# Performance work log

Measured on AMD Instinct MI355X. Metric: run time of the kernel, lower is better.

## Reference

```python
import jax, jax.numpy as jnp
import numpy as np

ALPHA = 0.2  # LeakyReLU negative slope

def setup_inputs() -> dict:
    key = jax.random.key(0)
    kx, kw, kb, ka = jax.random.split(key, 4)
    B, K, D, H = 4, 256, 128, 4
    x = jax.random.normal(kx, (B, K, D), dtype=jnp.float32)
    # Per-head Linear(2D -> D): stored as (H, 2D, D), i.e. transposed torch layout (y = v @ W + b)
    W = jax.random.normal(kw, (H, 2 * D, D), dtype=jnp.float32) * (1.0 / np.sqrt(2 * D))
    lin_b = jax.random.normal(kb, (H, D), dtype=jnp.float32) * 0.01
    # Per-head attention vector a: (H, D)
    a = jax.random.normal(ka, (H, D), dtype=jnp.float32) * (1.0 / np.sqrt(D))
    # Per-head additive bias over attention logits, initialized to zeros like the torch module
    bias = jnp.zeros((H, K, K), dtype=jnp.float32)
    return {"x": x, "W": W, "lin_b": lin_b, "a": a, "bias": bias}

def reference(x, W, lin_b, a, bias):
    # GATv2, dense all-pairs attention over K nodes, eval mode (dropout off).
    # Faithful decomposition: Linear(concat(x_i, x_j)) == x_i @ W_src + x_j @ W_dst + b
    B, K, D = x.shape
    H = W.shape[0]
    outs = []
    for h in range(H):  # small fixed head count; each head has distinct params
        W_src, W_dst = W[h, :D], W[h, D:]          # (D, D) each
        left = x @ W_src                            # (B, K, D) -> contribution of node i
        right = x @ W_dst                           # (B, K, D) -> contribution of node j
        s = left[:, :, None, :] + right[:, None, :, :] + lin_b[h]  # (B, K, K, D)
        s = jnp.where(s > 0, s, ALPHA * s)          # LeakyReLU
        e = jnp.einsum('bijd,d->bij', s, a[h]) + bias[h]           # (B, K, K)
        attn = jax.nn.softmax(e, axis=2)
        outs.append(attn @ x)                       # (B, K, D)
    return jnp.mean(jnp.stack(outs, axis=-1), axis=-1)
```

## Files before the change

kernel.cpp:

```cpp
#include <hip/hip_runtime.h>
#include <math.h>

constexpr int Kc = 256, Dc = 128, Mc = 1024;

typedef _Float16 h2_t __attribute__((ext_vector_type(2)));
union U32H2 { unsigned int u; h2_t h; };
__device__ inline h2_t u2h(unsigned int u) { U32H2 x; x.u = u; return x.h; }
__device__ inline unsigned int h2u(h2_t h) { U32H2 x; x.h = h; return x.u; }
__device__ inline unsigned int packh(float a, float b) {
    h2_t h; h.x = (_Float16)a; h.y = (_Float16)b; return h2u(h);
}
__device__ inline unsigned int f2bf(float f) {
    unsigned int u = __float_as_uint(f);
    return (u + 0x7FFFu + ((u >> 16) & 1u)) >> 16;
}
__device__ inline float bf2f_lo(unsigned int u) { return __uint_as_float(u << 16); }
__device__ inline float bf2f_hi(unsigned int u) { return __uint_as_float(u & 0xFFFF0000u); }

__device__ inline float estep(unsigned int r, unsigned int l, h2_t av, float acc) {
    h2_t s = u2h(r) + u2h(l);
    unsigned int t = h2u(s) & 0x7FFF7FFFu;
#if __has_builtin(__builtin_amdgcn_fdot2)
    return __builtin_amdgcn_fdot2(u2h(t), av, acc, false);
#else
    h2_t th = u2h(t);
    return fmaf((float)th.x, (float)av.x, fmaf((float)th.y, (float)av.y, acc));
#endif
}

__global__ __launch_bounds__(256) void k1(const float* __restrict__ x,
                                          const float* __restrict__ W,
                                          const float* __restrict__ lin_b,
                                          const float* __restrict__ a,
                                          unsigned int* __restrict__ Lpp,
                                          unsigned int* __restrict__ Rtp,
                                          float* __restrict__ eb) {
    __shared__ float As[128][32];
    __shared__ float Bs[128][64];
    __shared__ float red[4][16][4];

    const int tid = threadIdx.x;
    const int bid = blockIdx.x;
    const int tx = tid & 15, ty = tid >> 4;
    const bool isL = (bid < 256);

    int h, b, m0, n0, dt;
    if (isL) {
        const int nt = bid & 1, mt = (bid >> 1) & 31;
        h = (bid >> 6) & 3;
        m0 = mt * 32; n0 = nt * 64; b = 0; dt = 0;
        {
            const int m_l = tid & 31, kq = tid >> 5;
            #pragma unroll
            for (int c = 0; c < 4; ++c) {
                const int k0 = kq * 16 + c * 4;
                const float4 v = *(const float4*)&x[(m0 + m_l) * Dc + k0];
                As[k0 + 0][m_l] = v.x; As[k0 + 1][m_l] = v.y;
                As[k0 + 2][m_l] = v.z; As[k0 + 3][m_l] = v.w;
            }
        }
        {
            const int n_l = tid & 63, kq = tid >> 6;
            const float* Wb = W + (h * 2) * Dc * Dc;
            #pragma unroll
            for (int kk = 0; kk < 32; ++kk) {
                const int k = kq * 32 + kk;
                Bs[k][n_l] = Wb[k * Dc + n0 + n_l];
            }
        }
    } else {
        const int r_ = bid - 256;
        const int jt = r_ & 3;
        dt = (r_ >> 2) & 3;
        b  = (r_ >> 4) & 3;
        h  = (r_ >> 6) & 3;
        m0 = dt * 32;
        n0 = jt * 64;
        {
            const int d_l = tid & 31, kq = tid >> 5;
            const float* Wb = W + ((h * 2 + 1) * Dc) * Dc;
            #pragma unroll
            for (int kk = 0; kk < 16; ++kk) {
                const int k = kq * 16 + kk;
                As[k][d_l] = Wb[k * Dc + m0 + d_l];
            }
        }
        {
            const int j_l = tid & 63, kq = tid >> 6;
            #pragma unroll
            for (int c = 0; c < 8; ++c) {
                const int k0 = kq * 32 + c * 4;
                const float4 v = *(const float4*)&x[(b * Kc + n0 + j_l) * Dc + k0];
                Bs[k0 + 0][j_l] = v.x; Bs[k0 + 1][j_l] = v.y;
                Bs[k0 + 2][j_l] = v.z; Bs[k0 + 3][j_l] = v.w;
            }
        }
    }
    __syncthreads();

    float acc[2][4];
    #pragma unroll
    for (int r = 0; r < 2; ++r)
        #pragma unroll
        for (int c = 0; c < 4; ++c) acc[r][c] = 0.f;

    #pragma unroll 16
    for (int k = 0; k < 128; ++k) {
        const float2 xa = *(const float2*)&As[k][ty * 2];
        const float4 wb = *(const float4*)&Bs[k][tx * 4];
        acc[0][0] = fmaf(xa.x, wb.x, acc[0][0]);
        acc[0][1] = fmaf(xa.x, wb.y, acc[0][1]);
        acc[0][2] = fmaf(xa.x, wb.z, acc[0][2]);
        acc[0][3] = fmaf(xa.x, wb.w, acc[0][3]);
        acc[1][0] = fmaf(xa.y, wb.x, acc[1][0]);
        acc[1][1] = fmaf(xa.y, wb.y, acc[1][1]);
        acc[1][2] = fmaf(xa.y, wb.z, acc[1][2]);
        acc[1][3] = fmaf(xa.y, wb.w, acc[1][3]);
    }

    if (isL) {
        const float4 lv = *(const float4*)&lin_b[h * Dc + n0 + tx * 4];
        #pragma unroll
        for (int r = 0; r < 2; ++r) {
            uint2 pk;
            pk.x = packh(acc[r][0] + lv.x, acc[r][1] + lv.y);
            pk.y = packh(acc[r][2] + lv.z, acc[r][3] + lv.w);
            *(uint2*)&Lpp[(h * Mc + m0 + ty * 2 + r) * 64 + (n0 >> 1) + tx * 2] = pk;
        }
    } else {
        {
            uint4 pk;
            pk.x = packh(acc[0][0], acc[1][0]);
            pk.y = packh(acc[0][1], acc[1][1]);
            pk.z = packh(acc[0][2], acc[1][2]);
            pk.w = packh(acc[0][3], acc[1][3]);
            *(uint4*)&Rtp[((h * 4 + b) * 64 + (m0 >> 1) + ty) * Kc + n0 + tx * 4] = pk;
        }
        const float2 av = *(const float2*)&a[h * Dc + m0 + ty * 2];
        float p0 = 0.4f * (av.x * acc[0][0] + av.y * acc[1][0]);
        float p1 = 0.4f * (av.x * acc[0][1] + av.y * acc[1][1]);
        float p2 = 0.4f * (av.x * acc[0][2] + av.y * acc[1][2]);
        float p3 = 0.4f * (av.x * acc[0][3] + av.y * acc[1][3]);
        p0 += __shfl_xor(p0, 16, 64); p0 += __shfl_xor(p0, 32, 64);
        p1 += __shfl_xor(p1, 16, 64); p1 += __shfl_xor(p1, 32, 64);
        p2 += __shfl_xor(p2, 16, 64); p2 += __shfl_xor(p2, 32, 64);
        p3 += __shfl_xor(p3, 16, 64); p3 += __shfl_xor(p3, 32, 64);
        if (((tid >> 4) & 3) == 0) {
            const int w = tid >> 6;
            red[w][tx][0] = p0; red[w][tx][1] = p1;
            red[w][tx][2] = p2; red[w][tx][3] = p3;
        }
        __syncthreads();
        if (tid < 64) {
            const int txl = tid >> 2, c = tid & 3;
            const float v = red[0][txl][c] + red[1][txl][c] + red[2][txl][c] + red[3][txl][c];
            eb[((h * 4 + b) * 4 + dt) * Kc + n0 + tid] = 1.5f * v;
        }
    }
}

__global__ __launch_bounds__(256) void k2(const float* __restrict__ a,
                                          const float* __restrict__ bias,
                                          const unsigned int* __restrict__ Lpp,
                                          const unsigned int* __restrict__ Rtp,
                                          const float* __restrict__ eb,
                                          unsigned short* __restrict__ Pws) {
    __shared__ float red[256 * 20];
    __shared__ unsigned int lpT2[64 * 4];
    __shared__ unsigned int aa2s[64];

    const int tid = threadIdx.x;
    const int L = blockIdx.x;
    const int xcd = L & 7, q = L >> 3;
    const int hb = (xcd << 1) | (q & 1);
    const int it = q >> 1;
    const int h = hb >> 2, b = hb & 3;
    const int i0 = it * 4;

    {
        const int i = tid & 3, dp = tid >> 2;
        lpT2[dp * 4 + i] = Lpp[(h * Mc + b * Kc + i0 + i) * 64 + dp];
    }
    if (tid < 64) aa2s[tid] = packh(0.4f * a[h * Dc + 2 * tid], 0.4f * a[h * Dc + 2 * tid + 1]);
    __syncthreads();

    const int dq = tid >> 6, j4 = tid & 63;
    float4 acc0 = make_float4(0.f, 0.f, 0.f, 0.f);
    float4 acc1 = make_float4(0.f, 0.f, 0.f, 0.f);
    float4 acc2 = make_float4(0.f, 0.f, 0.f, 0.f);
    float4 acc3 = make_float4(0.f, 0.f, 0.f, 0.f);
    {
        const unsigned int* rb = Rtp + (hb * 64 + dq * 16) * Kc + j4 * 4;
        const unsigned int* lt = lpT2 + dq * 16 * 4;
        const unsigned int* at = aa2s + dq * 16;
        #pragma unroll
        for (int dp = 0; dp < 16; ++dp) {
            const uint4 rr = *(const uint4*)(rb + dp * Kc);
            const uint4 lp = *(const uint4*)(lt + dp * 4);
            const h2_t av = u2h(at[dp]);
            acc0.x = estep(rr.x, lp.x, av, acc0.x);
            acc0.y = estep(rr.y, lp.x, av, acc0.y);
            acc0.z = estep(rr.z, lp.x, av, acc0.z);
            acc0.w = estep(rr.w, lp.x, av, acc0.w);
            acc1.x = estep(rr.x, lp.y, av, acc1.x);
            acc1.y = estep(rr.y, lp.y, av, acc1.y);
            acc1.z = estep(rr.z, lp.y, av, acc1.z);
            acc1.w = estep(rr.w, lp.y, av, acc1.w);
            acc2.x = estep(rr.x, lp.z, av, acc2.x);
            acc2.y = estep(rr.y, lp.z, av, acc2.y);
            acc2.z = estep(rr.z, lp.z, av, acc2.z);
            acc2.w = estep(rr.w, lp.z, av, acc2.w);
            acc3.x = estep(rr.x, lp.w, av, acc3.x);
            acc3.y = estep(rr.y, lp.w, av, acc3.y);
            acc3.z = estep(rr.z, lp.w, av, acc3.z);
            acc3.w = estep(rr.w, lp.w, av, acc3.w);
        }
    }
    {
        float* myred = red + tid * 20;
        *(float4*)&myred[0]  = acc0;
        *(float4*)&myred[4]  = acc1;
        *(float4*)&myred[8]  = acc2;
        *(float4*)&myred[12] = acc3;
    }
    __syncthreads();

    {
        const int w = tid >> 6, l = tid & 63;
        float4 e0 = make_float4(0.f, 0.f, 0.f, 0.f);
        #pragma unroll
        for (int q4 = 0; q4 < 4; ++q4) {
            const float4 v = *(const float4*)&red[(q4 * 64 + l) * 20 + w * 4];
            e0.x += v.x; e0.y += v.y; e0.z += v.z; e0.w += v.w;
        }
        float4 ebs = make_float4(0.f, 0.f, 0.f, 0.f);
        #pragma unroll
        for (int seg = 0; seg < 4; ++seg) {
            const float4 v = *(const float4*)&eb[(hb * 4 + seg) * Kc + l * 4];
            ebs.x += v.x; ebs.y += v.y; ebs.z += v.z; ebs.w += v.w;
        }
        const float4 bv = *(const float4*)&bias[(h * Kc + i0 + w) * Kc + l * 4];
        e0.x += ebs.x + bv.x;
        e0.y += ebs.y + bv.y;
        e0.z += ebs.z + bv.z;
        e0.w += ebs.w + bv.w;

        float m = fmaxf(fmaxf(e0.x, e0.y), fmaxf(e0.z, e0.w));
        #pragma unroll
        for (int off = 1; off < 64; off <<= 1) m = fmaxf(m, __shfl_xor(m, off, 64));
        const float p0 = __expf(e0.x - m), p1 = __expf(e0.y - m);
        const float p2 = __expf(e0.z - m), p3 = __expf(e0.w - m);
        float s = p0 + p1 + p2 + p3;
        #pragma unroll
        for (int off = 1; off < 64; off <<= 1) s += __shfl_xor(s, off, 64);
        const float sc = 0.25f / s;
        uint2 pk;
        pk.x = f2bf(p0 * sc) | (f2bf(p1 * sc) << 16);
        pk.y = f2bf(p2 * sc) | (f2bf(p3 * sc) << 16);
        *(uint2*)&Pws[(hb * Kc + i0 + w) * Kc + l * 4] = pk;
    }
}

__global__ __launch_bounds__(256) void k3(const float* __restrict__ x,
                                          const unsigned short* __restrict__ Pws,
                                          float* __restrict__ out) {
    __shared__ float pbar[2 * Kc];
    __shared__ float red[256 * 12];

    const int tid = threadIdx.x;
    const int bid = blockIdx.x;
    const int b = bid >> 7, it = bid & 127;
    const int i0 = it * 2;

    if (tid < 128) {
        const int r = tid >> 6, c = tid & 63;
        float4 s = make_float4(0.f, 0.f, 0.f, 0.f);
        #pragma unroll
        for (int h = 0; h < 4; ++h) {
            const uint2 v = *(const uint2*)&Pws[((h * 4 + b) * Kc + i0 + r) * Kc + c * 4];
            s.x += bf2f_lo(v.x); s.y += bf2f_hi(v.x);
            s.z += bf2f_lo(v.y); s.w += bf2f_hi(v.y);
        }
        *(float4*)&pbar[r * Kc + c * 4] = s;
    }
    __syncthreads();

    const int jq = tid >> 5, dd4 = tid & 31;
    float4 o0 = make_float4(0.f, 0.f, 0.f, 0.f);
    float4 o1 = make_float4(0.f, 0.f, 0.f, 0.f);
    {
        const float* xb = x + (b * Kc) * Dc + dd4 * 4;
        #pragma unroll 4
        for (int jj = 0; jj < 32; ++jj) {
            const int j = jj * 8 + jq;
            const float4 xv = *(const float4*)(xb + j * Dc);
            const float pv0 = pbar[j];
            const float pv1 = pbar[Kc + j];
            o0.x = fmaf(pv0, xv.x, o0.x); o0.y = fmaf(pv0, xv.y, o0.y);
            o0.z = fmaf(pv0, xv.z, o0.z); o0.w = fmaf(pv0, xv.w, o0.w);
            o1.x = fmaf(pv1, xv.x, o1.x); o1.y = fmaf(pv1, xv.y, o1.y);
            o1.z = fmaf(pv1, xv.z, o1.z); o1.w = fmaf(pv1, xv.w, o1.w);
        }
    }
    {
        float* myred = red + (jq * 32 + dd4) * 12;
        *(float4*)&myred[0] = o0;
        *(float4*)&myred[4] = o1;
    }
    __syncthreads();
    if (tid < 64) {
        const int i_f = tid >> 5, dd_f = tid & 31;
        float4 s = make_float4(0.f, 0.f, 0.f, 0.f);
        #pragma unroll
        for (int q = 0; q < 8; ++q) {
            const float4 v = *(const float4*)&red[(q * 32 + dd_f) * 12 + i_f * 4];
            s.x += v.x; s.y += v.y; s.z += v.z; s.w += v.w;
        }
        *(float4*)&out[(b * Kc + i0 + i_f) * Dc + dd_f * 4] = s;
    }
}

extern "C" void kernel_launch(void* const* d_in, const int* in_sizes, int n_in,
                              void* d_out, int out_size, void* d_ws, size_t ws_size,
                              hipStream_t stream) {
    const float* x     = (const float*)d_in[0];
    const float* W     = (const float*)d_in[1];
    const float* lin_b = (const float*)d_in[2];
    const float* a     = (const float*)d_in[3];
    const float* bias  = (const float*)d_in[4];
    float* out = (float*)d_out;

    unsigned int*   Lpp = (unsigned int*)d_ws;
    unsigned int*   Rtp = Lpp + 4 * Mc * 64;
    float*          eb  = (float*)(Rtp + 16 * 64 * Kc);
    unsigned short* Pws = (unsigned short*)(eb + 16384);

    k1<<<512, 256, 0, stream>>>(x, W, lin_b, a, Lpp, Rtp, eb);
    k2<<<1024, 256, 0, stream>>>(a, bias, Lpp, Rtp, eb, Pws);
    k3<<<512, 256, 0, stream>>>(x, Pws, out);
}
```

Baseline: 26.74 us.

## Fuse attention softmax and aggregation kernels, loop heads per block

```diff
diff --git a/kernel.cpp b/kernel.cpp
--- a/kernel.cpp
+++ b/kernel.cpp
@@ -10,12 +10,6 @@
 __device__ inline unsigned int packh(float a, float b) {
     h2_t h; h.x = (_Float16)a; h.y = (_Float16)b; return h2u(h);
 }
-__device__ inline unsigned int f2bf(float f) {
-    unsigned int u = __float_as_uint(f);
-    return (u + 0x7FFFu + ((u >> 16) & 1u)) >> 16;
-}
-__device__ inline float bf2f_lo(unsigned int u) { return __uint_as_float(u << 16); }
-__device__ inline float bf2f_hi(unsigned int u) { return __uint_as_float(u & 0xFFFF0000u); }
 
 __device__ inline float estep(unsigned int r, unsigned int l, h2_t av, float acc) {
     h2_t s = u2h(r) + u2h(l);
@@ -159,131 +153,107 @@
     }
 }
 
-__global__ __launch_bounds__(256) void k2(const float* __restrict__ a,
+#define E4(ACC, LPV)                               \
+    ACC.x = estep(rr.x, LPV, av, ACC.x);           \
+    ACC.y = estep(rr.y, LPV, av, ACC.y);           \
+    ACC.z = estep(rr.z, LPV, av, ACC.z);           \
+    ACC.w = estep(rr.w, LPV, av, ACC.w);
+
+__global__ __launch_bounds__(256) void k2(const float* __restrict__ x,
+                                          const float* __restrict__ a,
                                           const float* __restrict__ bias,
                                           const unsigned int* __restrict__ Lpp,
                                           const unsigned int* __restrict__ Rtp,
                                           const float* __restrict__ eb,
-                                          unsigned short* __restrict__ Pws) {
-    __shared__ float red[256 * 20];
-    __shared__ unsigned int lpT2[64 * 4];
-    __shared__ unsigned int aa2s[64];
+                                          float* __restrict__ out) {
+    __shared__ float red[256 * 12];
+    __shared__ unsigned int lpT2[4 * 64 * 2];
+    __shared__ unsigned int aa2s[4 * 64];
+    __shared__ float plbar[2 * Kc];
 
     const int tid = threadIdx.x;
     const int L = blockIdx.x;
-    const int xcd = L & 7, q = L >> 3;
-    const int hb = (xcd << 1) | (q & 1);
-    const int it = q >> 1;
-    const int h = hb >> 2, b = hb & 3;
-    const int i0 = it * 4;
+    const int xcd = L & 7;
+    const int b = xcd >> 1;
+    const int it = ((L >> 3) << 1) | (xcd & 1);
+    const int i0 = it * 2;
 
     {
-        const int i = tid & 3, dp = tid >> 2;
-        lpT2[dp * 4 + i] = Lpp[(h * Mc + b * Kc + i0 + i) * 64 + dp];
-    }
-    if (tid < 64) aa2s[tid] = packh(0.4f * a[h * Dc + 2 * tid], 0.4f * a[h * Dc + 2 * tid + 1]);
+        const int h = tid >> 6, dp = tid & 63;
+        uint2 v;
+        v.x = Lpp[(h * Mc + b * Kc + i0 + 0) * 64 + dp];
+        v.y = Lpp[(h * Mc + b * Kc + i0 + 1) * 64 + dp];
+        *(uint2*)&lpT2[(h * 64 + dp) * 2] = v;
+        aa2s[tid] = packh(0.4f * a[h * Dc + 2 * dp], 0.4f * a[h * Dc + 2 * dp + 1]);
+    }
+    if (tid < 128) ((float4*)plbar)[tid] = make_float4(0.f, 0.f, 0.f, 0.f);
     __syncthreads();
 
     const int dq = tid >> 6, j4 = tid & 63;
-    float4 acc0 = make_float4(0.f, 0.f, 0.f, 0.f);
-    float4 acc1 = make_float4(0.f, 0.f, 0.f, 0.f);
-    float4 acc2 = make_float4(0.f, 0.f, 0.f, 0.f);
-    float4 acc3 = make_float4(0.f, 0.f, 0.f, 0.f);
-    {
-        const unsigned int* rb = Rtp + (hb * 64 + dq * 16) * Kc + j4 * 4;
-        const unsigned int* lt = lpT2 + dq * 16 * 4;
-        const unsigned int* at = aa2s + dq * 16;
-        #pragma unroll
-        for (int dp = 0; dp < 16; ++dp) {
-            const uint4 rr = *(const uint4*)(rb + dp * Kc);
-            const uint4 lp = *(const uint4*)(lt + dp * 4);
-            const h2_t av = u2h(at[dp]);
-            acc0.x = estep(rr.x, lp.x, av, acc0.x);
-            acc0.y = estep(rr.y, lp.x, av, acc0.y);
-            acc0.z = estep(rr.z, lp.x, av, acc0.z);
-            acc0.w = estep(rr.w, lp.x, av, acc0.w);
-            acc1.x = estep(rr.x, lp.y, av, acc1.x);
-            acc1.y = estep(rr.y, lp.y, av, acc1.y);
-            acc1.z = estep(rr.z, lp.y, av, acc1.z);
-            acc1.w = estep(rr.w, lp.y, av, acc1.w);
-            acc2.x = estep(rr.x, lp.z, av, acc2.x);
-            acc2.y = estep(rr.y, lp.z, av, acc2.y);
-            acc2.z = estep(rr.z, lp.z, av, acc2.z);
-            acc2.w = estep(rr.w, lp.z, av, acc2.w);
-            acc3.x = estep(rr.x, lp.w, av, acc3.x);
-            acc3.y = estep(rr.y, lp.w, av, acc3.y);
-            acc3.z = estep(rr.z, lp.w, av, acc3.z);
-            acc3.w = estep(rr.w, lp.w, av, acc3.w);
-        }
-    }
-    {
-        float* myred = red + tid * 20;
-        *(float4*)&myred[0]  = acc0;
-        *(float4*)&myred[4]  = acc1;
-        *(float4*)&myred[8]  = acc2;
-        *(float4*)&myred[12] = acc3;
-    }
-    __syncthreads();
-
-    {
-        const int w = tid >> 6, l = tid & 63;
-        float4 e0 = make_float4(0.f, 0.f, 0.f, 0.f);
-        #pragma unroll
-        for (int q4 = 0; q4 < 4; ++q4) {
-            const float4 v = *(const float4*)&red[(q4 * 64 + l) * 20 + w * 4];
-            e0.x += v.x; e0.y += v.y; e0.z += v.z; e0.w += v.w;
-        }
-        float4 ebs = make_float4(0.f, 0.f, 0.f, 0.f);
-        #pragma unroll
-        for (int seg = 0; seg < 4; ++seg) {
-            const float4 v = *(const float4*)&eb[(hb * 4 + seg) * Kc + l * 4];
-            ebs.x += v.x; ebs.y += v.y; ebs.z += v.z; ebs.w += v.w;
-        }
-        const float4 bv = *(const float4*)&bias[(h * Kc + i0 + w) * Kc + l * 4];
-        e0.x += ebs.x + bv.x;
-        e0.y += ebs.y + bv.y;
-        e0.z += ebs.z + bv.z;
-        e0.w += ebs.w + bv.w;
-
-        float m = fmaxf(fmaxf(e0.x, e0.y), fmaxf(e0.z, e0.w));
-        #pragma unroll
-        for (int off = 1; off < 64; off <<= 1) m = fmaxf(m, __shfl_xor(m, off, 64));
-        const float p0 = __expf(e0.x - m), p1 = __expf(e0.y - m);
-        const float p2 = __expf(e0.z - m), p3 = __expf(e0.w - m);
-        float s = p0 + p1 + p2 + p3;
-        #pragma unroll
-        for (int off = 1; off < 64; off <<= 1) s += __shfl_xor(s, off, 64);
-        const float sc = 0.25f / s;
-        uint2 pk;
-        pk.x = f2bf(p0 * sc) | (f2bf(p1 * sc) << 16);
-        pk.y = f2bf(p2 * sc) | (f2bf(p3 * sc) << 16);
-        *(uint2*)&Pws[(hb * Kc + i0 + w) * Kc + l * 4] = pk;
-    }
-}
-
-__global__ __launch_bounds__(256) void k3(const float* __restrict__ x,
-                                          const unsigned short* __restrict__ Pws,
-                                          float* __restrict__ out) {
-    __shared__ float pbar[2 * Kc];
-    __shared__ float red[256 * 12];
-
-    const int tid = threadIdx.x;
-    const int bid = blockIdx.x;
-    const int b = bid >> 7, it = bid & 127;
-    const int i0 = it * 2;
-
-    if (tid < 128) {
-        const int r = tid >> 6, c = tid & 63;
-        float4 s = make_float4(0.f, 0.f, 0.f, 0.f);
-        #pragma unroll
-        for (int h = 0; h < 4; ++h) {
-            const uint2 v = *(const uint2*)&Pws[((h * 4 + b) * Kc + i0 + r) * Kc + c * 4];
-            s.x += bf2f_lo(v.x); s.y += bf2f_hi(v.x);
-            s.z += bf2f_lo(v.y); s.w += bf2f_hi(v.y);
-        }
-        *(float4*)&pbar[r * Kc + c * 4] = s;
-    }
-    __syncthreads();
+    const int w = tid >> 6, l = tid & 63;
+
+    #pragma unroll 1
+    for (int h = 0; h < 4; ++h) {
+        const int hb = h * 4 + b;
+        float4 acc0 = make_float4(0.f, 0.f, 0.f, 0.f);
+        float4 acc1 = make_float4(0.f, 0.f, 0.f, 0.f);
+        {
+            const unsigned int* rb = Rtp + (hb * 64 + dq * 16) * Kc + j4 * 4;
+            const unsigned int* lt = lpT2 + (h * 64 + dq * 16) * 2;
+            const unsigned int* at = aa2s + h * 64 + dq * 16;
+            #pragma unroll
+            for (int dp = 0; dp < 16; ++dp) {
+                const uint4 rr = *(const uint4*)(rb + dp * Kc);
+                const uint2 lp2 = *(const uint2*)(lt + dp * 2);
+                const h2_t av = u2h(at[dp]);
+                E4(acc0, lp2.x);
+                E4(acc1, lp2.y);
+            }
+        }
+        {
+            float* myred = red + tid * 12;
+            *(float4*)&myred[0] = acc0;
+            *(float4*)&myred[4] = acc1;
+        }
+        __syncthreads();
+
+        if (w < 2) {
+            float4 e0 = make_float4(0.f, 0.f, 0.f, 0.f);
+            #pragma unroll
+            for (int q4 = 0; q4 < 4; ++q4) {
+                const float4 v = *(const float4*)&red[(q4 * 64 + l) * 12 + w * 4];
+                e0.x += v.x; e0.y += v.y; e0.z += v.z; e0.w += v.w;
+            }
+            float4 ebs = make_float4(0.f, 0.f, 0.f, 0.f);
+            #pragma unroll
+            for (int seg = 0; seg < 4; ++seg) {
+                const float4 v = *(const float4*)&eb[(hb * 4 + seg) * Kc + l * 4];
+                ebs.x += v.x; ebs.y += v.y; ebs.z += v.z; ebs.w += v.w;
+            }
+            const float4 bv = *(const float4*)&bias[(h * Kc + i0 + w) * Kc + l * 4];
+            e0.x += ebs.x + bv.x;
+            e0.y += ebs.y + bv.y;
+            e0.z += ebs.z + bv.z;
+            e0.w += ebs.w + bv.w;
+
+            float m = fmaxf(fmaxf(e0.x, e0.y), fmaxf(e0.z, e0.w));
+            #pragma unroll
+            for (int off = 1; off < 64; off <<= 1) m = fmaxf(m, __shfl_xor(m, off, 64));
+            const float p0 = __expf(e0.x - m), p1 = __expf(e0.y - m);
+            const float p2 = __expf(e0.z - m), p3 = __expf(e0.w - m);
+            float s = p0 + p1 + p2 + p3;
+            #pragma unroll
+            for (int off = 1; off < 64; off <<= 1) s += __shfl_xor(s, off, 64);
+            const float sc = 0.25f / s;
+            float4 cur = *(float4*)&plbar[w * Kc + l * 4];
+            cur.x = fmaf(p0, sc, cur.x);
+            cur.y = fmaf(p1, sc, cur.y);
+            cur.z = fmaf(p2, sc, cur.z);
+            cur.w = fmaf(p3, sc, cur.w);
+            *(float4*)&plbar[w * Kc + l * 4] = cur;
+        }
+        __syncthreads();
+    }
 
     const int jq = tid >> 5, dd4 = tid & 31;
     float4 o0 = make_float4(0.f, 0.f, 0.f, 0.f);
@@ -294,8 +264,8 @@
         for (int jj = 0; jj < 32; ++jj) {
             const int j = jj * 8 + jq;
             const float4 xv = *(const float4*)(xb + j * Dc);
-            const float pv0 = pbar[j];
-            const float pv1 = pbar[Kc + j];
+            const float pv0 = plbar[j];
+            const float pv1 = plbar[Kc + j];
             o0.x = fmaf(pv0, xv.x, o0.x); o0.y = fmaf(pv0, xv.y, o0.y);
             o0.z = fmaf(pv0, xv.z, o0.z); o0.w = fmaf(pv0, xv.w, o0.w);
             o1.x = fmaf(pv1, xv.x, o1.x); o1.y = fmaf(pv1, xv.y, o1.y);
@@ -333,9 +303,7 @@
     unsigned int*   Lpp = (unsigned int*)d_ws;
     unsigned int*   Rtp = Lpp + 4 * Mc * 64;
     float*          eb  = (float*)(Rtp + 16 * 64 * Kc);
-    unsigned short* Pws = (unsigned short*)(eb + 16384);
 
     k1<<<512, 256, 0, stream>>>(x, W, lin_b, a, Lpp, Rtp, eb);
-    k2<<<1024, 256, 0, stream>>>(a, bias, Lpp, Rtp, eb, Pws);
-    k3<<<512, 256, 0, stream>>>(x, Pws, out);
-}
+    k2<<<512, 256, 0, stream>>>(x, a, bias, Lpp, Rtp, eb, out);
+}
```

New measurement: 26.43 us. No clear change (-1.2%).
